# Kernel optimization log

Measured on AMD Instinct MI355X. Metric: run time of the kernel, lower is better.

The kernel has to match this reference:

```python
import jax, jax.numpy as jnp
import numpy as np

IN_DIM, OUT_DIM = 256, 64
N_D, N_G, N_C, N_S = 100000, 50000, 50000, 20000
E = 1000000
ALPHA = 0.2  # LeakyReLU negative slope


def setup_inputs() -> dict:
    key = jax.random.key(0)
    ks = jax.random.split(key, 14)
    scale = float(np.sqrt(6.0 / (IN_DIM + OUT_DIM)) * 1.414)
    scale_w = float(np.sqrt(6.0 / (4 * OUT_DIM + OUT_DIM)) * 1.414)
    return {
        "disease_feats": jax.random.normal(ks[0], (N_D, IN_DIM), jnp.float32),
        "gene_feats": jax.random.normal(ks[1], (N_G, IN_DIM), jnp.float32),
        "chemical_feats": jax.random.normal(ks[2], (N_C, IN_DIM), jnp.float32),
        "species_feats": jax.random.normal(ks[3], (N_S, IN_DIM), jnp.float32),
        "P_disease": jax.random.uniform(ks[4], (IN_DIM, OUT_DIM), jnp.float32, -scale, scale),
        "P_gene": jax.random.uniform(ks[5], (IN_DIM, OUT_DIM), jnp.float32, -scale, scale),
        "P_chemical": jax.random.uniform(ks[6], (IN_DIM, OUT_DIM), jnp.float32, -scale, scale),
        "P_species": jax.random.uniform(ks[7], (IN_DIM, OUT_DIM), jnp.float32, -scale, scale),
        "W_GDCD": jax.random.uniform(ks[8], (4 * OUT_DIM, OUT_DIM), jnp.float32, -scale_w, scale_w),
        "idx_d0": jax.random.randint(ks[9], (E,), 0, N_D, jnp.int32),
        "idx_d1": jax.random.randint(ks[10], (E,), 0, N_D, jnp.int32),
        "idx_g": jax.random.randint(ks[11], (E,), 0, N_G, jnp.int32),
        "idx_c": jax.random.randint(ks[12], (E,), 0, N_C, jnp.int32),
    }


def reference(disease_feats, gene_feats, chemical_feats, species_feats,
              P_disease, P_gene, P_chemical, P_species, W_GDCD,
              idx_d0, idx_d1, idx_g, idx_c):
    # Per-type linear projections (pattern 'GDCD')
    f_disease = disease_feats @ P_disease      # [N_D, out]
    f_gene = gene_feats @ P_gene               # [N_G, out]
    f_chemical = chemical_feats @ P_chemical   # [N_C, out]
    # f_species is computed by the torch code but unused for GDCD; omitted (dead code under jit)
    # Gather per-instance rows and concat -> [E, 4*out]
    concat = jnp.concatenate(
        [f_disease[idx_d0], f_disease[idx_d1], f_gene[idx_g], f_chemical[idx_c]], axis=1)
    instance = concat @ W_GDCD                 # [E, out]
    return jax.nn.leaky_relu(instance, negative_slope=ALPHA)
```

## Files before the change

kernel.cpp:

```cpp
#include <hip/hip_runtime.h>

typedef __attribute__((ext_vector_type(8))) short          short8;
typedef __attribute__((ext_vector_type(4))) float          f32x4;
typedef __attribute__((ext_vector_type(8))) unsigned short ushort8;

#define ALPHA 0.2f

__device__ __forceinline__ unsigned short f2bf(float f) {
    union { float f; unsigned int u; } x; x.f = f;
    unsigned int u = x.u;
    u += 0x7fffu + ((u >> 16) & 1u);
    return (unsigned short)(u >> 16);
}
__device__ __forceinline__ float bf2f(unsigned short u) {
    union { unsigned int i; float f; } x; x.i = ((unsigned int)u) << 16;
    return x.f;
}

__global__ __launch_bounds__(256)
void make_frags(const float* __restrict__ Pd, const float* __restrict__ Pg,
                const float* __restrict__ Pc, const float* __restrict__ W,
                unsigned short* __restrict__ fd, unsigned short* __restrict__ fg,
                unsigned short* __restrict__ fc) {
    int t = blockIdx.x * 256 + threadIdx.x;
    int local, NCT, mbase; unsigned short* dst;
    if (t < 32768)      { local = t;         NCT = 8; dst = fd; mbase = 0; }
    else if (t < 49152) { local = t - 32768; NCT = 4; dst = fg; mbase = 2; }
    else                { local = t - 49152; NCT = 4; dst = fc; mbase = 3; }
    int j    = local & 7;
    int lane = (local >> 3) & 63;
    int ct   = (local >> 9) & (NCT - 1);
    int kk   = local >> (9 + (NCT == 8 ? 3 : 2));
    int k = kk * 32 + ((lane >> 4) << 3) + j;
    int c = ct * 16 + (lane & 15);
    int m, cc; const float* P;
    if (NCT == 8) { m = (c < 64) ? 0 : 1; cc = c & 63; P = Pd; }
    else          { m = mbase;            cc = c;      P = (mbase == 2) ? Pg : Pc; }
    float acc = 0.f;
    #pragma unroll 8
    for (int q = 0; q < 64; ++q)
        acc += P[k * 64 + q] * W[(m * 64 + q) * 64 + cc];
    dst[local] = f2bf(acc);
}

template <int NCT>
__device__ __forceinline__
void proj_body(const float* __restrict__ feats,
               const unsigned short* __restrict__ bfrag,
               unsigned short* __restrict__ g, int ntiles, int blk,
               unsigned short* blds) {
    const int t = threadIdx.x;
    #pragma unroll
    for (int i = 0; i < NCT; ++i) {
        int off = (i * 512 + t) * 8;
        *(int4*)&blds[off] = *(const int4*)&bfrag[off];
    }
    __syncthreads();

    const int wid = t >> 6, lane = t & 63;
    const int C = NCT * 16;
    const int tile = blk * 8 + wid;
    if (tile >= ntiles) return;

    const int row = tile * 16 + (lane & 15);
    const float* arow = feats + (size_t)row * 256 + ((lane >> 4) * 8);

    f32x4 acc[NCT];
    #pragma unroll
    for (int ct = 0; ct < NCT; ++ct) acc[ct] = (f32x4){0.f, 0.f, 0.f, 0.f};

    #pragma unroll
    for (int kk = 0; kk < 8; ++kk) {
        f32x4 v0 = *(const f32x4*)(arow + kk * 32);
        f32x4 v1 = *(const f32x4*)(arow + kk * 32 + 4);
        short8 a;
        a[0] = (short)f2bf(v0[0]); a[1] = (short)f2bf(v0[1]);
        a[2] = (short)f2bf(v0[2]); a[3] = (short)f2bf(v0[3]);
        a[4] = (short)f2bf(v1[0]); a[5] = (short)f2bf(v1[1]);
        a[6] = (short)f2bf(v1[2]); a[7] = (short)f2bf(v1[3]);
        #pragma unroll
        for (int ct = 0; ct < NCT; ++ct) {
            short8 b = *(const short8*)&blds[((kk * NCT + ct) * 64 + lane) * 8];
            acc[ct] = __builtin_amdgcn_mfma_f32_16x16x32_bf16(a, b, acc[ct], 0, 0, 0);
        }
    }

    const int rbase = tile * 16 + (lane >> 4) * 4;
    const int cbase = lane & 15;
    #pragma unroll
    for (int ct = 0; ct < NCT; ++ct) {
        #pragma unroll
        for (int j = 0; j < 4; ++j)
            g[(size_t)(rbase + j) * C + ct * 16 + cbase] = f2bf(acc[ct][j]);
    }
}

__global__ __launch_bounds__(512)
void proj_all(const float* __restrict__ featd, const float* __restrict__ featg,
              const float* __restrict__ featc,
              const unsigned short* __restrict__ fragd,
              const unsigned short* __restrict__ fragg,
              const unsigned short* __restrict__ fragc,
              unsigned short* __restrict__ g_d, unsigned short* __restrict__ g_g,
              unsigned short* __restrict__ g_c,
              int nbd, int nbg, int td, int tg, int tc) {
    __shared__ unsigned short blds[32768];
    int b = blockIdx.x;
    if (b < nbd)            proj_body<8>(featd, fragd, g_d, td, b,             blds);
    else if (b < nbd + nbg) proj_body<4>(featg, fragg, g_g, tg, b - nbd,       blds);
    else                    proj_body<4>(featc, fragc, g_c, tc, b - nbd - nbg, blds);
}

__global__ __launch_bounds__(256)
void gather_kernel(const unsigned short* __restrict__ g_d,
                   const unsigned short* __restrict__ g_g,
                   const unsigned short* __restrict__ g_c,
                   const int* __restrict__ i0, const int* __restrict__ i1,
                   const int* __restrict__ ig, const int* __restrict__ ic,
                   float* __restrict__ out, int E) {
    int tid = blockIdx.x * 256 + threadIdx.x;
    int e = tid >> 3;
    if (e >= E) return;
    int q = tid & 7;

    int a  = __builtin_nontemporal_load(i0 + e);
    int b  = __builtin_nontemporal_load(i1 + e);
    int gi = __builtin_nontemporal_load(ig + e);
    int ci = __builtin_nontemporal_load(ic + e);

    ushort8 v0 = *(const ushort8*)(g_d + (size_t)a * 128 + q * 8);
    ushort8 v1 = *(const ushort8*)(g_d + (size_t)b * 128 + 64 + q * 8);
    ushort8 v2 = *(const ushort8*)(g_g + (size_t)gi * 64 + q * 8);
    ushort8 v3 = *(const ushort8*)(g_c + (size_t)ci * 64 + q * 8);

    f32x4 r0, r1;
    #pragma unroll
    for (int j = 0; j < 4; ++j) {
        float s = bf2f(v0[j]) + bf2f(v1[j]) + bf2f(v2[j]) + bf2f(v3[j]);
        r0[j] = s >= 0.f ? s : s * ALPHA;
        float u = bf2f(v0[j + 4]) + bf2f(v1[j + 4]) + bf2f(v2[j + 4]) + bf2f(v3[j + 4]);
        r1[j] = u >= 0.f ? u : u * ALPHA;
    }

    float* o = out + (size_t)e * 64 + q * 8;
    __builtin_nontemporal_store(r0, (f32x4*)o);
    __builtin_nontemporal_store(r1, (f32x4*)(o + 4));
}

extern "C" void kernel_launch(void* const* d_in, const int* in_sizes, int n_in,
                              void* d_out, int out_size, void* d_ws, size_t ws_size,
                              hipStream_t stream) {
    const float* feats_d = (const float*)d_in[0];
    const float* feats_g = (const float*)d_in[1];
    const float* feats_c = (const float*)d_in[2];
    const float* Pd = (const float*)d_in[4];
    const float* Pg = (const float*)d_in[5];
    const float* Pc = (const float*)d_in[6];
    const float* W  = (const float*)d_in[8];
    const int* i0 = (const int*)d_in[9];
    const int* i1 = (const int*)d_in[10];
    const int* ig = (const int*)d_in[11];
    const int* ic = (const int*)d_in[12];
    float* out = (float*)d_out;

    const int N_D = in_sizes[0] / 256;
    const int N_G = in_sizes[1] / 256;
    const int N_C = in_sizes[2] / 256;
    const int E   = in_sizes[9];

    char* ws = (char*)d_ws;
    unsigned short* fd  = (unsigned short*)ws;
    unsigned short* fg  = (unsigned short*)(ws + 65536);
    unsigned short* fc  = (unsigned short*)(ws + 98304);
    unsigned short* g_d = (unsigned short*)(ws + 131072);
    unsigned short* g_g = g_d + (size_t)N_D * 128;
    unsigned short* g_c = g_g + (size_t)N_G * 64;

    make_frags<<<256, 256, 0, stream>>>(Pd, Pg, Pc, W, fd, fg, fc);

    int td = N_D / 16, tg = N_G / 16, tc = N_C / 16;
    int nbd = (td + 7) / 8, nbg = (tg + 7) / 8, nbc = (tc + 7) / 8;
    proj_all<<<nbd + nbg + nbc, 512, 0, stream>>>(
        feats_d, feats_g, feats_c, fd, fg, fc, g_d, g_g, g_c,
        nbd, nbg, td, tg, tc);

    long long nthreads = (long long)E * 8;
    gather_kernel<<<(int)((nthreads + 255) / 256), 256, 0, stream>>>(
        g_d, g_g, g_c, i0, i1, ig, ic, out, E);
}
```

Baseline: 166.3 us.

## Fuse frag, projection and gather stages into one cooperative persistent kernel

Merges the three launches (fragment precompute, projection GEMM, gather-sum-LeakyReLU) into one cooperative kernel that uses grid-wide syncs between stages. The grid is persistent, sized from an occupancy query and capped at two blocks per CU, and it loops over projection tile groups and gather elements. B-fragment staging into shared memory is cached per type. The aim is to remove launch gaps and tail effects between kernels. The cost is grid.sync overhead and possibly lower parallelism in the first stage. If the cooperative launch fails, the old three-kernel path runs instead.

```diff
diff --git a/kernel.cpp b/kernel.cpp
--- a/kernel.cpp
+++ b/kernel.cpp
@@ -1,4 +1,7 @@
 #include <hip/hip_runtime.h>
+#include <hip/hip_cooperative_groups.h>
+
+namespace cg = cooperative_groups;
 
 typedef __attribute__((ext_vector_type(8))) short          short8;
 typedef __attribute__((ext_vector_type(4))) float          f32x4;
@@ -17,12 +20,11 @@
     return x.f;
 }
 
-__global__ __launch_bounds__(256)
-void make_frags(const float* __restrict__ Pd, const float* __restrict__ Pg,
-                const float* __restrict__ Pc, const float* __restrict__ W,
-                unsigned short* __restrict__ fd, unsigned short* __restrict__ fg,
-                unsigned short* __restrict__ fc) {
-    int t = blockIdx.x * 256 + threadIdx.x;
+__device__ __forceinline__
+void frag_element(int t, const float* __restrict__ Pd, const float* __restrict__ Pg,
+                  const float* __restrict__ Pc, const float* __restrict__ W,
+                  unsigned short* __restrict__ fd, unsigned short* __restrict__ fg,
+                  unsigned short* __restrict__ fc) {
     int local, NCT, mbase; unsigned short* dst;
     if (t < 32768)      { local = t;         NCT = 8; dst = fd; mbase = 0; }
     else if (t < 49152) { local = t - 32768; NCT = 4; dst = fg; mbase = 2; }
@@ -43,23 +45,22 @@
     dst[local] = f2bf(acc);
 }
 
+__device__ __forceinline__
+void stage_frags(const unsigned short* __restrict__ src, unsigned short* blds, int NCT) {
+    for (int i = 0; i < NCT; ++i) {
+        int off = (i * 512 + (int)threadIdx.x) * 8;
+        *(int4*)&blds[off] = *(const int4*)&src[off];
+    }
+}
+
 template <int NCT>
 __device__ __forceinline__
-void proj_body(const float* __restrict__ feats,
-               const unsigned short* __restrict__ bfrag,
-               unsigned short* __restrict__ g, int ntiles, int blk,
-               unsigned short* blds) {
+void proj_tile(const float* __restrict__ feats, unsigned short* __restrict__ g,
+               int ntiles, int lg, const unsigned short* blds) {
     const int t = threadIdx.x;
-    #pragma unroll
-    for (int i = 0; i < NCT; ++i) {
-        int off = (i * 512 + t) * 8;
-        *(int4*)&blds[off] = *(const int4*)&bfrag[off];
-    }
-    __syncthreads();
-
     const int wid = t >> 6, lane = t & 63;
     const int C = NCT * 16;
-    const int tile = blk * 8 + wid;
+    const int tile = lg * 8 + wid;
     if (tile >= ntiles) return;
 
     const int row = tile * 16 + (lane & 15);
@@ -95,32 +96,14 @@
     }
 }
 
-__global__ __launch_bounds__(512)
-void proj_all(const float* __restrict__ featd, const float* __restrict__ featg,
-              const float* __restrict__ featc,
-              const unsigned short* __restrict__ fragd,
-              const unsigned short* __restrict__ fragg,
-              const unsigned short* __restrict__ fragc,
-              unsigned short* __restrict__ g_d, unsigned short* __restrict__ g_g,
-              unsigned short* __restrict__ g_c,
-              int nbd, int nbg, int td, int tg, int tc) {
-    __shared__ unsigned short blds[32768];
-    int b = blockIdx.x;
-    if (b < nbd)            proj_body<8>(featd, fragd, g_d, td, b,             blds);
-    else if (b < nbd + nbg) proj_body<4>(featg, fragg, g_g, tg, b - nbd,       blds);
-    else                    proj_body<4>(featc, fragc, g_c, tc, b - nbd - nbg, blds);
-}
-
-__global__ __launch_bounds__(256)
-void gather_kernel(const unsigned short* __restrict__ g_d,
-                   const unsigned short* __restrict__ g_g,
-                   const unsigned short* __restrict__ g_c,
-                   const int* __restrict__ i0, const int* __restrict__ i1,
-                   const int* __restrict__ ig, const int* __restrict__ ic,
-                   float* __restrict__ out, int E) {
-    int tid = blockIdx.x * 256 + threadIdx.x;
+__device__ __forceinline__
+void gather_one(int tid, const unsigned short* __restrict__ g_d,
+                const unsigned short* __restrict__ g_g,
+                const unsigned short* __restrict__ g_c,
+                const int* __restrict__ i0, const int* __restrict__ i1,
+                const int* __restrict__ ig, const int* __restrict__ ic,
+                float* __restrict__ out) {
     int e = tid >> 3;
-    if (e >= E) return;
     int q = tid & 7;
 
     int a  = __builtin_nontemporal_load(i0 + e);
@@ -141,10 +124,99 @@
         float u = bf2f(v0[j + 4]) + bf2f(v1[j + 4]) + bf2f(v2[j + 4]) + bf2f(v3[j + 4]);
         r1[j] = u >= 0.f ? u : u * ALPHA;
     }
-
     float* o = out + (size_t)e * 64 + q * 8;
     __builtin_nontemporal_store(r0, (f32x4*)o);
     __builtin_nontemporal_store(r1, (f32x4*)(o + 4));
+}
+
+__global__ __launch_bounds__(512, 4)
+void fused(const float* featd, const float* featg, const float* featc,
+           const float* Pd, const float* Pg, const float* Pc, const float* W,
+           const int* i0, const int* i1, const int* ig, const int* ic,
+           float* out,
+           unsigned short* fd, unsigned short* fg, unsigned short* fc,
+           unsigned short* g_d, unsigned short* g_g, unsigned short* g_c,
+           int td, int tg, int tc, int nbd, int nbg, int nbc, int E) {
+    __shared__ unsigned short blds[32768];
+    cg::grid_group grid = cg::this_grid();
+    const int nthr = gridDim.x * 512;
+
+    {
+        int t = blockIdx.x * 512 + threadIdx.x;
+        if (t < 65536) frag_element(t, Pd, Pg, Pc, W, fd, fg, fc);
+    }
+    grid.sync();
+
+    {
+        const int ngroups = nbd + nbg + nbc;
+        int cached = -1;
+        for (int grp = blockIdx.x; grp < ngroups; grp += gridDim.x) {
+            int type, lg;
+            if (grp < nbd)            { type = 0; lg = grp; }
+            else if (grp < nbd + nbg) { type = 1; lg = grp - nbd; }
+            else                      { type = 2; lg = grp - nbd - nbg; }
+            if (type != cached) {
+                __syncthreads();
+                const unsigned short* src = (type == 0) ? fd : (type == 1 ? fg : fc);
+                stage_frags(src, blds, type == 0 ? 8 : 4);
+                __syncthreads();
+                cached = type;
+            }
+            if (type == 0)      proj_tile<8>(featd, g_d, td, lg, blds);
+            else if (type == 1) proj_tile<4>(featg, g_g, tg, lg, blds);
+            else                proj_tile<4>(featc, g_c, tc, lg, blds);
+        }
+    }
+    grid.sync();
+
+    {
+        const int total = E * 8;
+        for (int tid = blockIdx.x * 512 + (int)threadIdx.x; tid < total; tid += nthr)
+            gather_one(tid, g_d, g_g, g_c, i0, i1, ig, ic, out);
+    }
+}
+
+__global__ __launch_bounds__(256)
+void make_frags_k(const float* __restrict__ Pd, const float* __restrict__ Pg,
+                  const float* __restrict__ Pc, const float* __restrict__ W,
+                  unsigned short* __restrict__ fd, unsigned short* __restrict__ fg,
+                  unsigned short* __restrict__ fc) {
+    frag_element(blockIdx.x * 256 + threadIdx.x, Pd, Pg, Pc, W, fd, fg, fc);
+}
+
+__global__ __launch_bounds__(512)
+void proj_all_k(const float* __restrict__ featd, const float* __restrict__ featg,
+                const float* __restrict__ featc,
+                const unsigned short* __restrict__ fragd,
+                const unsigned short* __restrict__ fragg,
+                const unsigned short* __restrict__ fragc,
+                unsigned short* __restrict__ g_d, unsigned short* __restrict__ g_g,
+                unsigned short* __restrict__ g_c,
+                int nbd, int nbg, int td, int tg, int tc) {
+    __shared__ unsigned short blds[32768];
+    int b = blockIdx.x;
+    if (b < nbd) {
+        stage_frags(fragd, blds, 8); __syncthreads();
+        proj_tile<8>(featd, g_d, td, b, blds);
+    } else if (b < nbd + nbg) {
+        stage_frags(fragg, blds, 4); __syncthreads();
+        proj_tile<4>(featg, g_g, tg, b - nbd, blds);
+    } else {
+        stage_frags(fragc, blds, 4); __syncthreads();
+        proj_tile<4>(featc, g_c, tc, b - nbd - nbg, blds);
+    }
+}
+
+__global__ __launch_bounds__(256)
+void gather_k(const unsigned short* __restrict__ g_d,
+              const unsigned short* __restrict__ g_g,
+              const unsigned short* __restrict__ g_c,
+              const int* __restrict__ i0, const int* __restrict__ i1,
+              const int* __restrict__ ig, const int* __restrict__ ic,
+              float* __restrict__ out, int E) {
+    int tid = blockIdx.x * 256 + threadIdx.x;
+    if ((tid >> 3) >= E) return;
+    gather_one(tid, g_d, g_g, g_c, i0, i1, ig, ic, out);
 }
 
 extern "C" void kernel_launch(void* const* d_in, const int* in_sizes, int n_in,
@@ -166,7 +238,7 @@
     const int N_D = in_sizes[0] / 256;
     const int N_G = in_sizes[1] / 256;
     const int N_C = in_sizes[2] / 256;
-    const int E   = in_sizes[9];
+    int E = in_sizes[9];
 
     char* ws = (char*)d_ws;
     unsigned short* fd  = (unsigned short*)ws;
@@ -176,15 +248,35 @@
     unsigned short* g_g = g_d + (size_t)N_D * 128;
     unsigned short* g_c = g_g + (size_t)N_G * 64;
 
-    make_frags<<<256, 256, 0, stream>>>(Pd, Pg, Pc, W, fd, fg, fc);
-
     int td = N_D / 16, tg = N_G / 16, tc = N_C / 16;
     int nbd = (td + 7) / 8, nbg = (tg + 7) / 8, nbc = (tc + 7) / 8;
-    proj_all<<<nbd + nbg + nbc, 512, 0, stream>>>(
-        feats_d, feats_g, feats_c, fd, fg, fc, g_d, g_g, g_c,
-        nbd, nbg, td, tg, tc);
-
-    long long nthreads = (long long)E * 8;
-    gather_kernel<<<(int)((nthreads + 255) / 256), 256, 0, stream>>>(
-        g_d, g_g, g_c, i0, i1, ig, ic, out, E);
-}
+
+    int maxb = 0;
+    hipError_t qerr = hipOccupancyMaxActiveBlocksPerMultiprocessor(&maxb, fused, 512, 0);
+    if (qerr != hipSuccess || maxb < 1) maxb = 1;
+    if (maxb > 2) maxb = 2;
+    dim3 grid(maxb * 256), block(512);
+
+    void* kargs[] = {
+        (void*)&feats_d, (void*)&feats_g, (void*)&feats_c,
+        (void*)&Pd, (void*)&Pg, (void*)&Pc, (void*)&W,
+        (void*)&i0, (void*)&i1, (void*)&ig, (void*)&ic,
+        (void*)&out,
+        (void*)&fd, (void*)&fg, (void*)&fc,
+        (void*)&g_d, (void*)&g_g, (void*)&g_c,
+        (void*)&td, (void*)&tg, (void*)&tc,
+        (void*)&nbd, (void*)&nbg, (void*)&nbc, (void*)&E };
+
+    hipError_t err = hipLaunchCooperativeKernel((const void*)fused, grid, block,
+                                                kargs, 0u, stream);
+    if (err != hipSuccess) {
+        (void)hipGetLastError();
+        make_frags_k<<<256, 256, 0, stream>>>(Pd, Pg, Pc, W, fd, fg, fc);
+        proj_all_k<<<nbd + nbg + nbc, 512, 0, stream>>>(
+            feats_d, feats_g, feats_c, fd, fg, fc, g_d, g_g, g_c,
+            nbd, nbg, td, tg, tc);
+        long long nthreads = (long long)E * 8;
+        gather_k<<<(int)((nthreads + 255) / 256), 256, 0, stream>>>(
+            g_d, g_g, g_c, i0, i1, ig, ic, out, E);
+    }
+}
```

After: 231.9 us. 39.4% more time.
